# Performance work log

Hardware: AMD Instinct MI355X
Metric: run time of the kernel (lower is better)

## Reference

```python
import jax, jax.numpy as jnp
import numpy as np

INPUT_DIM = 128
HIDDEN_DIM = 64
BATCH = 256
SEQ_LEN = 1024


def _projectors(n):
    n_half = n // 2
    S = jnp.zeros((n, n), jnp.float32)
    S = S.at[:n_half, n_half:].set(jnp.eye(n_half))
    S = S.at[n_half:, :n_half].set(jnp.eye(n_half))
    I = jnp.eye(n, dtype=jnp.float32)
    return (I + S) / 2.0, (I - S) / 2.0


def setup_inputs() -> dict:
    key = jax.random.key(0)
    ks = jax.random.split(key, 7)
    x = jax.random.normal(ks[0], (BATCH, SEQ_LEN, INPUT_DIM), jnp.float32)
    A_plus = jax.random.normal(ks[1], (HIDDEN_DIM, HIDDEN_DIM), jnp.float32) * 0.1
    A_minus = jax.random.normal(ks[2], (HIDDEN_DIM, HIDDEN_DIM), jnp.float32) * 0.1
    # nn.Linear default init: U(-1/sqrt(fan_in), 1/sqrt(fan_in))
    b_in = 1.0 / np.sqrt(INPUT_DIM)
    W_in_w = jax.random.uniform(ks[3], (HIDDEN_DIM, INPUT_DIM), jnp.float32, -b_in, b_in)
    W_in_b = jax.random.uniform(ks[4], (HIDDEN_DIM,), jnp.float32, -b_in, b_in)
    b_out = 1.0 / np.sqrt(HIDDEN_DIM)
    W_out_w = jax.random.uniform(ks[5], (INPUT_DIM, HIDDEN_DIM), jnp.float32, -b_out, b_out)
    W_out_b = jax.random.uniform(ks[6], (INPUT_DIM,), jnp.float32, -b_out, b_out)
    bias = jnp.zeros((HIDDEN_DIM,), jnp.float32)
    return {"x": x, "A_plus": A_plus, "A_minus": A_minus,
            "W_in_w": W_in_w, "W_in_b": W_in_b,
            "W_out_w": W_out_w, "W_out_b": W_out_b, "bias": bias}


def reference(x, A_plus, A_minus, W_in_w, W_in_b, W_out_w, W_out_b, bias):
    B, T, _ = x.shape
    H = bias.shape[0]
    P_plus, P_minus = _projectors(H)
    # W_comm = P+ A+ P+ + P- A- P-
    W_comm = P_plus @ A_plus @ P_plus + P_minus @ A_minus @ P_minus
    # Precompute input projection for all timesteps (one big GEMM): (B,T,H)
    inp = jnp.einsum('bti,hi->bth', x, W_in_w) + W_in_b + bias
    inp_t = jnp.transpose(inp, (1, 0, 2))  # (T,B,H)

    def step(h, u_t):
        h = jnp.tanh(h @ W_comm.T + u_t)
        return h, None

    h0 = jnp.zeros((B, H), x.dtype)
    hidden, _ = jax.lax.scan(step, h0, inp_t)
    predictions = hidden @ W_out_w.T + W_out_b  # (B, input_dim)
    return predictions, hidden
```

## Files before the change

kernel.cpp:

```cpp
#include <hip/hip_runtime.h>
#include <hip/hip_bf16.h>

#define BB 256
#define TT 1024
#define II 128
#define HH 64

typedef float    f32x4_t __attribute__((ext_vector_type(4)));
typedef _Float16 h16x2   __attribute__((ext_vector_type(2)));
typedef _Float16 h16x4   __attribute__((ext_vector_type(4)));
typedef _Float16 h16x8   __attribute__((ext_vector_type(8)));
typedef __fp16   p16x2   __attribute__((ext_vector_type(2)));

union UH2 { unsigned u; h16x2 h; p16x2 p; };
union U4H8 { uint4 u; h16x8 h; };

__device__ __forceinline__ float tanh_fast(float x){
  float e = __builtin_amdgcn_exp2f(x * 2.88539004f);
  return __builtin_fmaf(-2.0f, __builtin_amdgcn_rcpf(1.0f + e), 1.0f);
}

#if __has_builtin(__builtin_amdgcn_fdot2)
__device__ __forceinline__ float fdot2f(h16x2 a, h16x2 b, float c){
  return __builtin_amdgcn_fdot2(a, b, c, false);
}
#else
__device__ __forceinline__ float fdot2f(h16x2 a, h16x2 b, float c){
  return __builtin_fmaf((float)a[1], (float)b[1], __builtin_fmaf((float)a[0], (float)b[0], c));
}
#endif

__global__ void k_prep(const float* __restrict__ Ap, const float* __restrict__ Am,
                       const float* __restrict__ Winw,
                       const float* __restrict__ Winb, const float* __restrict__ bias,
                       float* __restrict__ wsf, unsigned* __restrict__ whf,
                       unsigned short* __restrict__ wsb){
  const int tid = threadIdx.x;
  for (int e = tid; e < 4096; e += 256){
    int i = e >> 6, j = e & 63;
    int is = i ^ 32, js = j ^ 32;
    float wp = Ap[i*64+j] + Ap[i*64+js] + Ap[is*64+j] + Ap[is*64+js];
    float wm = Am[i*64+j] - Am[i*64+js] - Am[is*64+j] + Am[is*64+js];
    wsf[e] = 0.25f * (wp + wm);
  }
  if (tid < 64) wsf[4096 + tid] = Winb[tid] + bias[tid];
  for (int e = tid; e < 8192; e += 256){
    int j = e & 7, lane = (e >> 3) & 63, fidx = e >> 9;
    int ks = fidx >> 2, nt = fidx & 3, l15 = lane & 15, q = lane >> 4;
    union { _Float16 f; unsigned short s; } cv;
    cv.f = (_Float16)Winw[(nt*16 + l15)*II + ks*32 + q*8 + j];
    wsb[e] = cv.s;
  }
  __syncthreads();
  for (int e = tid; e < 2048; e += 256){
    int i = e >> 5, jp = e & 31;
    UH2 p;
    p.h[0] = (_Float16)wsf[i*64 + 2*jp];
    p.h[1] = (_Float16)wsf[i*64 + 2*jp + 1];
    whf[e] = p.u;
  }
}

__global__ __launch_bounds__(256, 1) void k_fused(const float* __restrict__ x,
                                                  const float* __restrict__ wsf,
                                                  const unsigned* __restrict__ whf,
                                                  const unsigned short* __restrict__ wsb,
                                                  const float* __restrict__ Wout,
                                                  const float* __restrict__ Woutb,
                                                  float* __restrict__ out){
  extern __shared__ unsigned char smem[];
  unsigned short* Us    = (unsigned short*)smem;
  unsigned*       flags = (unsigned*)(smem + 131072);

  const int b    = blockIdx.x;
  const int tid  = threadIdx.x;
  const int lane = tid & 63;
  const int wave = tid >> 6;
  const int l15  = lane & 15;
  const int q    = lane >> 4;

  if (tid < 64) flags[tid] = 0u;
  __syncthreads();

  if (wave != 0){
    h16x8 bfr[4][4];
    #pragma unroll
    for (int ks = 0; ks < 4; ++ks)
      #pragma unroll
      for (int nt = 0; nt < 4; ++nt)
        bfr[ks][nt] = *(const h16x8*)(wsb + ((ks*4 + nt)*64 + lane)*8);

    float bcv[4];
    #pragma unroll
    for (int nt = 0; nt < 4; ++nt) bcv[nt] = wsf[4096 + nt*16 + l15];

    const float* xb = x + (long)b * (TT * II);

    #pragma unroll 1
    for (int tile = wave - 1; tile < 64; tile += 3){
      const int trow = tile * 16;
      const float* xa = xb + (trow + l15) * II + q*8;
      h16x8 afr[4];
      #pragma unroll
      for (int ks = 0; ks < 4; ++ks){
        float4 a0 = *(const float4*)(xa + ks*32);
        float4 a1 = *(const float4*)(xa + ks*32 + 4);
        U4H8 v;
        UH2 p0, p1, p2, p3;
        p0.p = __builtin_amdgcn_cvt_pkrtz(a0.x, a0.y);
        p1.p = __builtin_amdgcn_cvt_pkrtz(a0.z, a0.w);
        p2.p = __builtin_amdgcn_cvt_pkrtz(a1.x, a1.y);
        p3.p = __builtin_amdgcn_cvt_pkrtz(a1.z, a1.w);
        v.u.x = p0.u; v.u.y = p1.u; v.u.z = p2.u; v.u.w = p3.u;
        afr[ks] = v.h;
      }
      f32x4_t acc[4];
      #pragma unroll
      for (int nt = 0; nt < 4; ++nt){
        acc[nt][0]=bcv[nt]; acc[nt][1]=bcv[nt]; acc[nt][2]=bcv[nt]; acc[nt][3]=bcv[nt];
      }
      #pragma unroll
      for (int ks = 0; ks < 4; ++ks){
        #pragma unroll
        for (int nt = 0; nt < 4; ++nt){
          acc[nt] = __builtin_amdgcn_mfma_f32_16x16x32_f16(afr[ks], bfr[ks][nt], acc[nt], 0, 0, 0);
        }
      }
      const int tg = tile*4 + q;
      #pragma unroll
      for (int nt = 0; nt < 4; ++nt){
        UH2 lo, hi;
        lo.p = __builtin_amdgcn_cvt_pkrtz(acc[nt][0], acc[nt][1]);
        hi.p = __builtin_amdgcn_cvt_pkrtz(acc[nt][2], acc[nt][3]);
        uint2 pk; pk.x = lo.u; pk.y = hi.u;
        *(uint2*)&Us[(tg*64 + nt*16 + l15) * 4] = pk;
      }
      __threadfence_block();
      if (lane == 0)
        __hip_atomic_store(&flags[tile], 1u, __ATOMIC_RELEASE, __HIP_MEMORY_SCOPE_WORKGROUP);
    }
    return;
  }

  h16x2 w[32];
  {
    const uint4* wr = (const uint4*)(whf + lane * 32);
    #pragma unroll
    for (int j4 = 0; j4 < 8; ++j4){
      uint4 v = wr[j4];
      UH2 c0, c1, c2, c3;
      c0.u = v.x; c1.u = v.y; c2.u = v.z; c3.u = v.w;
      w[4*j4+0] = c0.h; w[4*j4+1] = c1.h; w[4*j4+2] = c2.h; w[4*j4+3] = c3.h;
    }
  }

  while (!__hip_atomic_load(&flags[0], __ATOMIC_ACQUIRE, __HIP_MEMORY_SCOPE_WORKGROUP)) {}

  const h16x4* Ul = (const h16x4*)Us;
  h16x4 uc = Ul[0*64 + lane];
  h16x4 u1 = Ul[1*64 + lane];

  float h = 0.0f;
  int last_ready = 0;
  #pragma unroll 1
  for (int tile = 0; tile < 64; ++tile){
    int wt = tile + 1; if (wt > 63) wt = 63;
    if (wt > last_ready){
      while (!__hip_atomic_load(&flags[wt], __ATOMIC_ACQUIRE, __HIP_MEMORY_SCOPE_WORKGROUP)) {}
      last_ready = wt;
    }
    #pragma unroll
    for (int tgl = 0; tgl < 4; ++tgl){
      const int tg = tile*4 + tgl;
      int tp = tg + 2; if (tp > TT/4 - 1) tp = TT/4 - 1;
      h16x4 u2 = Ul[tp*64 + lane];
      float ug0 = (float)uc[0], ug1 = (float)uc[1], ug2 = (float)uc[2], ug3 = (float)uc[3];
      #pragma unroll
      for (int g = 0; g < 4; ++g){
        float ugv = (g==0) ? ug0 : (g==1) ? ug1 : (g==2) ? ug2 : ug3;
        unsigned nbu = (unsigned)__builtin_amdgcn_mov_dpp(__float_as_uint(h), 0xB1, 0xF, 0xF, true);
        UH2 hp; hp.p = __builtin_amdgcn_cvt_pkrtz(h, __uint_as_float(nbu));
        const unsigned hpu = hp.u;
        float a0 = ugv, a1 = 0.0f, a2 = 0.0f, a3 = 0.0f;
        #pragma unroll
        for (int jp = 0; jp < 32; jp += 4){
          UH2 b0, b1, b2, b3;
          b0.u = (unsigned)__builtin_amdgcn_readlane(hpu, 2*jp + 0);
          b1.u = (unsigned)__builtin_amdgcn_readlane(hpu, 2*jp + 2);
          b2.u = (unsigned)__builtin_amdgcn_readlane(hpu, 2*jp + 4);
          b3.u = (unsigned)__builtin_amdgcn_readlane(hpu, 2*jp + 6);
          a0 = fdot2f(w[jp+0], b0.h, a0);
          a1 = fdot2f(w[jp+1], b1.h, a1);
          a2 = fdot2f(w[jp+2], b2.h, a2);
          a3 = fdot2f(w[jp+3], b3.h, a3);
        }
        h = tanh_fast((a0 + a1) + (a2 + a3));
      }
      uc = u1; u1 = u2;
    }
  }

  unsigned hu = __float_as_uint(h);
  float p0 = Woutb[lane];
  float p1 = Woutb[lane + 64];
  #pragma unroll 8
  for (int j = 0; j < 64; ++j){
    float hj = __uint_as_float(__builtin_amdgcn_readlane(hu, j));
    p0 = __builtin_fmaf(Wout[lane * HH + j],        hj, p0);
    p1 = __builtin_fmaf(Wout[(lane + 64) * HH + j], hj, p1);
  }
  out[b * 128 + lane]           = p0;
  out[b * 128 + 64 + lane]      = p1;
  out[BB * 128 + b * 64 + lane] = h;
}

extern "C" void kernel_launch(void* const* d_in, const int* in_sizes, int n_in,
                              void* d_out, int out_size, void* d_ws, size_t ws_size,
                              hipStream_t stream){
  const float* x     = (const float*)d_in[0];
  const float* Ap    = (const float*)d_in[1];
  const float* Am    = (const float*)d_in[2];
  const float* Winw  = (const float*)d_in[3];
  const float* Winb  = (const float*)d_in[4];
  const float* Woutw = (const float*)d_in[5];
  const float* Woutb = (const float*)d_in[6];
  const float* bias  = (const float*)d_in[7];

  float*          wsf = (float*)d_ws;
  unsigned*       whf = (unsigned*)((char*)d_ws + 16640);
  unsigned short* wsb = (unsigned short*)((char*)d_ws + 24832);

  float* out = (float*)d_out;

  hipFuncSetAttribute((const void*)k_fused,
                      hipFuncAttributeMaxDynamicSharedMemorySize, 131328);

  hipLaunchKernelGGL(k_prep,  dim3(1),   dim3(256), 0,      stream, Ap, Am, Winw, Winb, bias, wsf, whf, wsb);
  hipLaunchKernelGGL(k_fused, dim3(BB),  dim3(256), 131328, stream, x, wsf, whf, wsb, Woutw, Woutb, out);
}
```

Baseline: 330.3 us.

## Pack two batch rows per block with ring-buffered inputs and prescaled tanh

Each 512-thread block now handles two batch sequences, with one recurrence wave and three producer waves per sequence. The LDS input buffer per sequence becomes a 32-tile ring, and producers wait on a consumer progress counter before overwriting slots. This halves the grid, so the 256 recurrences can run at once with two per CU instead of spread over twice as many one-wave blocks. Separately, the 2/ln2 factor of tanh is folded into the weights and biases, which removes a multiply from the serial recurrence. The risks are the extra flow-control spinning and the fp16 range of the prescaled inputs.

```diff
diff --git a/kernel.cpp b/kernel.cpp
--- a/kernel.cpp
+++ b/kernel.cpp
@@ -5,6 +5,8 @@
 #define TT 1024
 #define II 128
 #define HH 64
+
+#define PRESCALE 2.8853900817779268f
 
 typedef float    f32x4_t __attribute__((ext_vector_type(4)));
 typedef _Float16 h16x2   __attribute__((ext_vector_type(2)));
@@ -15,8 +17,8 @@
 union UH2 { unsigned u; h16x2 h; p16x2 p; };
 union U4H8 { uint4 u; h16x8 h; };
 
-__device__ __forceinline__ float tanh_fast(float x){
-  float e = __builtin_amdgcn_exp2f(x * 2.88539004f);
+__device__ __forceinline__ float tanh_pre(float a){
+  float e = __builtin_amdgcn_exp2f(a);
   return __builtin_fmaf(-2.0f, __builtin_amdgcn_rcpf(1.0f + e), 1.0f);
 }
 
@@ -41,14 +43,14 @@
     int is = i ^ 32, js = j ^ 32;
     float wp = Ap[i*64+j] + Ap[i*64+js] + Ap[is*64+j] + Ap[is*64+js];
     float wm = Am[i*64+j] - Am[i*64+js] - Am[is*64+j] + Am[is*64+js];
-    wsf[e] = 0.25f * (wp + wm);
-  }
-  if (tid < 64) wsf[4096 + tid] = Winb[tid] + bias[tid];
+    wsf[e] = 0.25f * (wp + wm) * PRESCALE;
+  }
+  if (tid < 64) wsf[4096 + tid] = (Winb[tid] + bias[tid]) * PRESCALE;
   for (int e = tid; e < 8192; e += 256){
     int j = e & 7, lane = (e >> 3) & 63, fidx = e >> 9;
     int ks = fidx >> 2, nt = fidx & 3, l15 = lane & 15, q = lane >> 4;
     union { _Float16 f; unsigned short s; } cv;
-    cv.f = (_Float16)Winw[(nt*16 + l15)*II + ks*32 + q*8 + j];
+    cv.f = (_Float16)(Winw[(nt*16 + l15)*II + ks*32 + q*8 + j] * PRESCALE);
     wsb[e] = cv.s;
   }
   __syncthreads();
@@ -61,7 +63,7 @@
   }
 }
 
-__global__ __launch_bounds__(256, 1) void k_fused(const float* __restrict__ x,
+__global__ __launch_bounds__(512, 1) void k_fused(const float* __restrict__ x,
                                                   const float* __restrict__ wsf,
                                                   const unsigned* __restrict__ whf,
                                                   const unsigned short* __restrict__ wsb,
@@ -71,18 +73,22 @@
   extern __shared__ unsigned char smem[];
   unsigned short* Us    = (unsigned short*)smem;
   unsigned*       flags = (unsigned*)(smem + 131072);
-
-  const int b    = blockIdx.x;
+  unsigned*       cons  = flags + 128;
+
   const int tid  = threadIdx.x;
   const int lane = tid & 63;
   const int wave = tid >> 6;
   const int l15  = lane & 15;
   const int q    = lane >> 4;
-
-  if (tid < 64) flags[tid] = 0u;
+  const int sel  = (wave >= 4) ? 1 : 0;
+
+  if (tid < 130) flags[tid] = 0u;
   __syncthreads();
 
-  if (wave != 0){
+  unsigned* flg = flags + sel*64;
+
+  if ((wave & 3) != 0){
+    const int p = (wave & 3) - 1;
     h16x8 bfr[4][4];
     #pragma unroll
     for (int ks = 0; ks < 4; ++ks)
@@ -94,10 +100,14 @@
     #pragma unroll
     for (int nt = 0; nt < 4; ++nt) bcv[nt] = wsf[4096 + nt*16 + l15];
 
-    const float* xb = x + (long)b * (TT * II);
+    const float* xb = x + (long)(2*blockIdx.x + sel) * (TT * II);
+    unsigned short* Ub = Us + sel * 32768;
 
     #pragma unroll 1
-    for (int tile = wave - 1; tile < 64; tile += 3){
+    for (int tile = p; tile < 64; tile += 3){
+      if (tile > 30){
+        while (__hip_atomic_load(&cons[sel], __ATOMIC_ACQUIRE, __HIP_MEMORY_SCOPE_WORKGROUP) + 30u < (unsigned)tile) {}
+      }
       const int trow = tile * 16;
       const float* xa = xb + (trow + l15) * II + q*8;
       h16x8 afr[4];
@@ -126,18 +136,18 @@
           acc[nt] = __builtin_amdgcn_mfma_f32_16x16x32_f16(afr[ks], bfr[ks][nt], acc[nt], 0, 0, 0);
         }
       }
-      const int tg = tile*4 + q;
+      const int tgs = (tile & 31)*4 + q;
       #pragma unroll
       for (int nt = 0; nt < 4; ++nt){
         UH2 lo, hi;
         lo.p = __builtin_amdgcn_cvt_pkrtz(acc[nt][0], acc[nt][1]);
         hi.p = __builtin_amdgcn_cvt_pkrtz(acc[nt][2], acc[nt][3]);
         uint2 pk; pk.x = lo.u; pk.y = hi.u;
-        *(uint2*)&Us[(tg*64 + nt*16 + l15) * 4] = pk;
+        *(uint2*)&Ub[(tgs*64 + nt*16 + l15) * 4] = pk;
       }
       __threadfence_block();
       if (lane == 0)
-        __hip_atomic_store(&flags[tile], 1u, __ATOMIC_RELEASE, __HIP_MEMORY_SCOPE_WORKGROUP);
+        __hip_atomic_store(&flg[tile], 1u, __ATOMIC_RELEASE, __HIP_MEMORY_SCOPE_WORKGROUP);
     }
     return;
   }
@@ -154,9 +164,9 @@
     }
   }
 
-  while (!__hip_atomic_load(&flags[0], __ATOMIC_ACQUIRE, __HIP_MEMORY_SCOPE_WORKGROUP)) {}
-
-  const h16x4* Ul = (const h16x4*)Us;
+  while (!__hip_atomic_load(&flg[0], __ATOMIC_ACQUIRE, __HIP_MEMORY_SCOPE_WORKGROUP)) {}
+
+  const h16x4* Ul = (const h16x4*)Us + sel * 8192;
   h16x4 uc = Ul[0*64 + lane];
   h16x4 u1 = Ul[1*64 + lane];
 
@@ -166,14 +176,14 @@
   for (int tile = 0; tile < 64; ++tile){
     int wt = tile + 1; if (wt > 63) wt = 63;
     if (wt > last_ready){
-      while (!__hip_atomic_load(&flags[wt], __ATOMIC_ACQUIRE, __HIP_MEMORY_SCOPE_WORKGROUP)) {}
+      while (!__hip_atomic_load(&flg[wt], __ATOMIC_ACQUIRE, __HIP_MEMORY_SCOPE_WORKGROUP)) {}
       last_ready = wt;
     }
     #pragma unroll
     for (int tgl = 0; tgl < 4; ++tgl){
       const int tg = tile*4 + tgl;
       int tp = tg + 2; if (tp > TT/4 - 1) tp = TT/4 - 1;
-      h16x4 u2 = Ul[tp*64 + lane];
+      h16x4 u2 = Ul[(tp & 127)*64 + lane];
       float ug0 = (float)uc[0], ug1 = (float)uc[1], ug2 = (float)uc[2], ug3 = (float)uc[3];
       #pragma unroll
       for (int g = 0; g < 4; ++g){
@@ -194,12 +204,15 @@
           a2 = fdot2f(w[jp+2], b2.h, a2);
           a3 = fdot2f(w[jp+3], b3.h, a3);
         }
-        h = tanh_fast((a0 + a1) + (a2 + a3));
+        h = tanh_pre((a0 + a1) + (a2 + a3));
       }
       uc = u1; u1 = u2;
     }
-  }
-
+    if (lane == 0)
+      __hip_atomic_store(&cons[sel], (unsigned)(tile + 1), __ATOMIC_RELEASE, __HIP_MEMORY_SCOPE_WORKGROUP);
+  }
+
+  const int b = 2*blockIdx.x + sel;
   unsigned hu = __float_as_uint(h);
   float p0 = Woutb[lane];
   float p1 = Woutb[lane + 64];
@@ -233,8 +246,8 @@
   float* out = (float*)d_out;
 
   hipFuncSetAttribute((const void*)k_fused,
-                      hipFuncAttributeMaxDynamicSharedMemorySize, 131328);
-
-  hipLaunchKernelGGL(k_prep,  dim3(1),   dim3(256), 0,      stream, Ap, Am, Winw, Winb, bias, wsf, whf, wsb);
-  hipLaunchKernelGGL(k_fused, dim3(BB),  dim3(256), 131328, stream, x, wsf, whf, wsb, Woutw, Woutb, out);
-}
+                      hipFuncAttributeMaxDynamicSharedMemorySize, 131592);
+
+  hipLaunchKernelGGL(k_prep,  dim3(1),      dim3(256), 0,      stream, Ap, Am, Winw, Winb, bias, wsf, whf, wsb);
+  hipLaunchKernelGGL(k_fused, dim3(BB/2),   dim3(512), 131592, stream, x, wsf, whf, wsb, Woutw, Woutb, out);
+}
```

Result: slower. 465.6 us (+40.9%).

## Broadcast hidden state via LDS and fold tanh scale into weights

Applied to the files above, without the earlier changes.

Each step of the serial recurrence now writes the packed fp16 hidden pairs to a small LDS buffer and reads them back as eight 128-bit vector loads. This replaces 32 readlane instructions per step, which are scalar-path operations with latency on the critical chain. The exp2 prescale constant is folded into W_comm, the bias and W_in during prep, which removes one multiply per tanh. The cost is an LDS store/load round trip per step, relying on single-wave ordering with no barrier, plus fp16 rounding of weights that are now larger in magnitude.

```diff
diff --git a/kernel.cpp b/kernel.cpp
--- a/kernel.cpp
+++ b/kernel.cpp
@@ -5,6 +5,8 @@
 #define TT 1024
 #define II 128
 #define HH 64
+
+#define PRESCALE 2.8853900817779268f
 
 typedef float    f32x4_t __attribute__((ext_vector_type(4)));
 typedef _Float16 h16x2   __attribute__((ext_vector_type(2)));
@@ -14,9 +16,10 @@
 
 union UH2 { unsigned u; h16x2 h; p16x2 p; };
 union U4H8 { uint4 u; h16x8 h; };
-
-__device__ __forceinline__ float tanh_fast(float x){
-  float e = __builtin_amdgcn_exp2f(x * 2.88539004f);
+union B128 { uint4 u; h16x2 h[4]; };
+
+__device__ __forceinline__ float tanh_pre(float a){
+  float e = __builtin_amdgcn_exp2f(a);
   return __builtin_fmaf(-2.0f, __builtin_amdgcn_rcpf(1.0f + e), 1.0f);
 }
 
@@ -41,14 +44,14 @@
     int is = i ^ 32, js = j ^ 32;
     float wp = Ap[i*64+j] + Ap[i*64+js] + Ap[is*64+j] + Ap[is*64+js];
     float wm = Am[i*64+j] - Am[i*64+js] - Am[is*64+j] + Am[is*64+js];
-    wsf[e] = 0.25f * (wp + wm);
-  }
-  if (tid < 64) wsf[4096 + tid] = Winb[tid] + bias[tid];
+    wsf[e] = 0.25f * (wp + wm) * PRESCALE;
+  }
+  if (tid < 64) wsf[4096 + tid] = (Winb[tid] + bias[tid]) * PRESCALE;
   for (int e = tid; e < 8192; e += 256){
     int j = e & 7, lane = (e >> 3) & 63, fidx = e >> 9;
     int ks = fidx >> 2, nt = fidx & 3, l15 = lane & 15, q = lane >> 4;
     union { _Float16 f; unsigned short s; } cv;
-    cv.f = (_Float16)Winw[(nt*16 + l15)*II + ks*32 + q*8 + j];
+    cv.f = (_Float16)(Winw[(nt*16 + l15)*II + ks*32 + q*8 + j] * PRESCALE);
     wsb[e] = cv.s;
   }
   __syncthreads();
@@ -71,6 +74,7 @@
   extern __shared__ unsigned char smem[];
   unsigned short* Us    = (unsigned short*)smem;
   unsigned*       flags = (unsigned*)(smem + 131072);
+  unsigned*       Hb    = (unsigned*)(smem + 131072 + 256);
 
   const int b    = blockIdx.x;
   const int tid  = threadIdx.x;
@@ -160,6 +164,8 @@
   h16x4 uc = Ul[0*64 + lane];
   h16x4 u1 = Ul[1*64 + lane];
 
+  const bool wlane = !(lane & 1);
+
   float h = 0.0f;
   int last_ready = 0;
   #pragma unroll 1
@@ -180,21 +186,22 @@
         float ugv = (g==0) ? ug0 : (g==1) ? ug1 : (g==2) ? ug2 : ug3;
         unsigned nbu = (unsigned)__builtin_amdgcn_mov_dpp(__float_as_uint(h), 0xB1, 0xF, 0xF, true);
         UH2 hp; hp.p = __builtin_amdgcn_cvt_pkrtz(h, __uint_as_float(nbu));
-        const unsigned hpu = hp.u;
+        if (wlane) Hb[lane >> 1] = hp.u;
+        __asm__ volatile("" ::: "memory");
+        __builtin_amdgcn_sched_barrier(0);
+        B128 hv[8];
+        const uint4* Hr = (const uint4*)Hb;
+        #pragma unroll
+        for (int r = 0; r < 8; ++r) hv[r].u = Hr[r];
         float a0 = ugv, a1 = 0.0f, a2 = 0.0f, a3 = 0.0f;
         #pragma unroll
         for (int jp = 0; jp < 32; jp += 4){
-          UH2 b0, b1, b2, b3;
-          b0.u = (unsigned)__builtin_amdgcn_readlane(hpu, 2*jp + 0);
-          b1.u = (unsigned)__builtin_amdgcn_readlane(hpu, 2*jp + 2);
-          b2.u = (unsigned)__builtin_amdgcn_readlane(hpu, 2*jp + 4);
-          b3.u = (unsigned)__builtin_amdgcn_readlane(hpu, 2*jp + 6);
-          a0 = fdot2f(w[jp+0], b0.h, a0);
-          a1 = fdot2f(w[jp+1], b1.h, a1);
-          a2 = fdot2f(w[jp+2], b2.h, a2);
-          a3 = fdot2f(w[jp+3], b3.h, a3);
+          a0 = fdot2f(w[jp+0], hv[(jp+0)>>2].h[(jp+0)&3], a0);
+          a1 = fdot2f(w[jp+1], hv[(jp+1)>>2].h[(jp+1)&3], a1);
+          a2 = fdot2f(w[jp+2], hv[(jp+2)>>2].h[(jp+2)&3], a2);
+          a3 = fdot2f(w[jp+3], hv[(jp+3)>>2].h[(jp+3)&3], a3);
         }
-        h = tanh_fast((a0 + a1) + (a2 + a3));
+        h = tanh_pre((a0 + a1) + (a2 + a3));
       }
       uc = u1; u1 = u2;
     }
@@ -233,8 +240,8 @@
   float* out = (float*)d_out;
 
   hipFuncSetAttribute((const void*)k_fused,
-                      hipFuncAttributeMaxDynamicSharedMemorySize, 131328);
+                      hipFuncAttributeMaxDynamicSharedMemorySize, 131456);
 
   hipLaunchKernelGGL(k_prep,  dim3(1),   dim3(256), 0,      stream, Ap, Am, Winw, Winb, bias, wsf, whf, wsb);
-  hipLaunchKernelGGL(k_fused, dim3(BB),  dim3(256), 131328, stream, x, wsf, whf, wsb, Woutw, Woutb, out);
-}
+  hipLaunchKernelGGL(k_fused, dim3(BB),  dim3(256), 131456, stream, x, wsf, whf, wsb, Woutw, Woutb, out);
+}
```

Measured after the change: 339.5 us. 2.8% more time.
